# Performance work log

Hardware: AMD Instinct MI355X
Metric: run time of the kernel (lower is better)

Reference implementation:

```python
import jax, jax.numpy as jnp
import numpy as np


def setup_inputs() -> dict:
    key = jax.random.key(0)
    ks = jax.random.split(key, 9)
    B, Cr, H, W = 16, 1024, 28, 28
    Cs, Hs, Ws = 256, 25, 25  # Hs == Ws so adaptive pool == mean over width
    Ci = 512
    return {
        "x_rgb": jax.random.normal(ks[0], (B, Cr, H, W), jnp.float32),
        "x_skel": jax.random.normal(ks[1], (B, Cs, Hs, Ws), jnp.float32),
        "Wq": jax.random.normal(ks[2], (Ci, Cr), jnp.float32) * (Cr ** -0.5),
        "bq": jax.random.normal(ks[3], (Ci,), jnp.float32) * 0.01,
        "Wk": jax.random.normal(ks[4], (Ci, Cs), jnp.float32) * (Cs ** -0.5),
        "bk": jax.random.normal(ks[5], (Ci,), jnp.float32) * 0.01,
        "Wv": jax.random.normal(ks[6], (Cr, Cs), jnp.float32) * (Cs ** -0.5),
        "bv": jax.random.normal(ks[7], (Cr,), jnp.float32) * 0.01,
        "gamma": jax.random.normal(ks[8], (1,), jnp.float32) * 0.1,
    }


def reference(x_rgb, x_skel, Wq, bq, Wk, bk, Wv, bv, gamma):
    B, Cr, H, W = x_rgb.shape
    Ws = x_skel.shape[3]
    # adaptive_avg_pool2d(x_skel, (Ws, 1)) with Hs == Ws -> mean over width
    pooled = jnp.mean(x_skel, axis=3)  # [B, Cs, Ws]
    # 1x1 conv projections as matmuls
    q = jnp.einsum('ic,bchw->bihw', Wq, x_rgb) + bq[None, :, None, None]
    q = q.reshape(B, -1, H * W).transpose(0, 2, 1)          # [B, HW, Ci]
    k = jnp.einsum('ic,bcs->bis', Wk, pooled) + bk[None, :, None]  # [B, Ci, Ws]
    energy = jnp.einsum('bni,bis->bns', q, k)               # [B, HW, Ws]
    attention = jax.nn.softmax(energy, axis=-1)             # [B, HW, Ws]
    v = jnp.einsum('rc,bcs->brs', Wv, pooled) + bv[None, :, None]  # [B, Cr, Ws]
    out = jnp.einsum('brs,bns->brn', v, attention)          # [B, Cr, HW]
    out = out.reshape(B, Cr, H, W)
    return gamma[0] * out + x_rgb
```

## Files before the change

kernel.cpp:

```cpp
#include <hip/hip_runtime.h>

#define BB 16
#define CR 1024
#define HWD 784
#define HW2 392
#define CS 256
#define SSZ 25
#define SP 28
#define CI 512
#define CSPLIT 8
#define CCHUNK 128
#define RSPLIT 32
#define RCHUNK 32
#define KC 4

#define OFF_POOLED 0
#define OFF_VP     102400
#define OFF_MP     561152
#define OFF_E0     1019904
#define OFF_ATT    1020304
#define OFF_EP     1333904
#define OFF_KK     1333904
#define OFF_P      1563280

__global__ __launch_bounds__(256) void k_pool(const float* __restrict__ xs,
                                              float* __restrict__ pooled) {
    __shared__ float buf[4][400];
    int wave = threadIdx.x >> 6, lane = threadIdx.x & 63;
    int r0 = blockIdx.x * 64 + wave * 16;
    const float4* src = (const float4*)(xs + (size_t)r0 * SSZ);
    float4* b4 = (float4*)buf[wave];
    b4[lane] = src[lane];
    if (lane < 36) b4[64 + lane] = src[64 + lane];
    __syncthreads();
    if (lane < 16) {
        const float* row = buf[wave] + lane * SSZ;
        float s = 0.f;
#pragma unroll
        for (int w = 0; w < SSZ; ++w) s += row[w];
        pooled[r0 + lane] = s * (1.0f / SSZ);
    }
}

template <int NS>
__device__ __forceinline__ void proj_body(const float* __restrict__ wrow,
                                          const float* __restrict__ pb, int s0,
                                          float bias, float* __restrict__ dst,
                                          bool zpad) {
    float acc[NS];
#pragma unroll
    for (int i = 0; i < NS; ++i) acc[i] = 0.f;
    const float4* w4 = (const float4*)wrow;
#pragma unroll 4
    for (int c4 = 0; c4 < CS / 4; ++c4) {
        float4 w = w4[c4];
        const float* p = pb + c4 * 4 * SSZ + s0;
#pragma unroll
        for (int i = 0; i < NS; ++i)
            acc[i] = fmaf(w.x, p[i],
                     fmaf(w.y, p[SSZ + i],
                     fmaf(w.z, p[2 * SSZ + i],
                     fmaf(w.w, p[3 * SSZ + i], acc[i]))));
    }
#pragma unroll
    for (int i = 0; i < NS; ++i) dst[s0 + i] = acc[i] + bias;
    if (zpad) { dst[25] = 0.f; dst[26] = 0.f; dst[27] = 0.f; }
}

__global__ __launch_bounds__(256) void k_kkv(const float* __restrict__ Wk,
                                             const float* __restrict__ Wv,
                                             const float* __restrict__ bk,
                                             const float* __restrict__ bv,
                                             const float* __restrict__ pooled,
                                             float* __restrict__ kk,
                                             float* __restrict__ vp) {
    int rb = blockIdx.x >> 2, sh = blockIdx.x & 3;
    int b = blockIdx.y;
    const float* pb = pooled + (size_t)b * CS * SSZ;
    const float* wrow;
    float bias;
    float* dst;
    if (rb < 2) {
        int i = rb * 256 + threadIdx.x;
        wrow = Wk + (size_t)i * CS;
        bias = bk[i];
        dst = kk + ((size_t)b * CI + i) * SP;
    } else {
        int r = (rb - 2) * 256 + threadIdx.x;
        wrow = Wv + (size_t)r * CS;
        bias = bv[r];
        dst = vp + ((size_t)b * CR + r) * SP;
    }
    int s0 = sh * 7;
    if (sh < 3) proj_body<7>(wrow, pb, s0, bias, dst, false);
    else        proj_body<4>(wrow, pb, s0, bias, dst, true);
}

__global__ __launch_bounds__(256) void k_Mpart(const float* __restrict__ Wq,
                                               const float* __restrict__ kk,
                                               float* __restrict__ P) {
    __shared__ __align__(16) float lds[128 * 8];
    int sh = blockIdx.x, kc = blockIdx.y, b = blockIdx.z;
    int t = threadIdx.x;
    int s0 = sh * 7;
    int i0 = kc * 128;
    const float* kkb = kk + (size_t)b * CI * SP;
#pragma unroll
    for (int q = 0; q < 4; ++q) {
        int d = t + 256 * q;
        lds[d] = kkb[(size_t)(i0 + (d >> 3)) * SP + s0 + (d & 7)];
    }
    __syncthreads();

    float acc[28];
#pragma unroll
    for (int e = 0; e < 28; ++e) acc[e] = 0.f;
    const float4* lds4 = (const float4*)lds;
#pragma unroll 4
    for (int i = 0; i < 128; ++i) {
        float4 w = *(const float4*)(Wq + (size_t)(i0 + i) * CR + 4 * t);
        float4 k0 = lds4[i * 2];
        float4 k1 = lds4[i * 2 + 1];
#pragma unroll
        for (int j = 0; j < 4; ++j) {
            float wj = j == 0 ? w.x : j == 1 ? w.y : j == 2 ? w.z : w.w;
            acc[j * 7 + 0] = fmaf(wj, k0.x, acc[j * 7 + 0]);
            acc[j * 7 + 1] = fmaf(wj, k0.y, acc[j * 7 + 1]);
            acc[j * 7 + 2] = fmaf(wj, k0.z, acc[j * 7 + 2]);
            acc[j * 7 + 3] = fmaf(wj, k0.w, acc[j * 7 + 3]);
            acc[j * 7 + 4] = fmaf(wj, k1.x, acc[j * 7 + 4]);
            acc[j * 7 + 5] = fmaf(wj, k1.y, acc[j * 7 + 5]);
            acc[j * 7 + 6] = fmaf(wj, k1.z, acc[j * 7 + 6]);
        }
    }
    float* dst = P + ((((size_t)kc * BB + b) * 4 + sh) * 256 + t) * 28;
#pragma unroll
    for (int m = 0; m < 7; ++m) {
        float4 o;
        o.x = acc[4 * m + 0]; o.y = acc[4 * m + 1];
        o.z = acc[4 * m + 2]; o.w = acc[4 * m + 3];
        *(float4*)(dst + 4 * m) = o;
    }
}

__global__ __launch_bounds__(256) void k_Mred(const float* __restrict__ P,
                                              float* __restrict__ Mp) {
    int id = blockIdx.x * 256 + threadIdx.x;
    int t = id & 255, sh = (id >> 8) & 3, b = id >> 10;
    const float* p0 = P + ((((size_t)b) * 4 + sh) * 256 + t) * 28;
    const size_t PL = (size_t)BB * 4 * 256 * 28;
    float v[28];
#pragma unroll
    for (int m = 0; m < 7; ++m) {
        float4 a = *(const float4*)(p0 + 4 * m);
        float4 b1 = *(const float4*)(p0 + PL + 4 * m);
        float4 c = *(const float4*)(p0 + 2 * PL + 4 * m);
        float4 d = *(const float4*)(p0 + 3 * PL + 4 * m);
        v[4 * m + 0] = a.x + b1.x + c.x + d.x;
        v[4 * m + 1] = a.y + b1.y + c.y + d.y;
        v[4 * m + 2] = a.z + b1.z + c.z + d.z;
        v[4 * m + 3] = a.w + b1.w + c.w + d.w;
    }
    int s0 = sh * 7;
    float* mb = Mp + ((size_t)b * CR + 4 * t) * SP + s0;
#pragma unroll
    for (int j = 0; j < 4; ++j)
#pragma unroll
        for (int u = 0; u < 7; ++u)
            mb[j * SP + u] = v[j * 7 + u];
}

__global__ __launch_bounds__(64) void k_e0(const float* __restrict__ bq,
                                           const float* __restrict__ kk,
                                           float* __restrict__ e0) {
    int s = blockIdx.x, b = blockIdx.y;
    int l = threadIdx.x;
    const float* kb = kk + (size_t)b * CI * SP;
    float a = 0.f;
#pragma unroll
    for (int k = 0; k < CI / 64; ++k) {
        int i = l + 64 * k;
        a = fmaf(bq[i], kb[(size_t)i * SP + s], a);
    }
#pragma unroll
    for (int off = 32; off > 0; off >>= 1) a += __shfl_down(a, off);
    if (l == 0) e0[b * SSZ + s] = a;
}

__global__ __launch_bounds__(64) void k_energy(const float* __restrict__ xr,
                                               const float* __restrict__ Mp,
                                               float* __restrict__ Ep) {
    __shared__ float ldsM[CCHUNK * SP];
    int lane = threadIdx.x;
    int b = blockIdx.y, ch = blockIdx.z;
    int cbeg = ch * CCHUNK;
    {
        const float4* src = (const float4*)(Mp + ((size_t)b * CR + cbeg) * SP);
        float4* dst = (float4*)ldsM;
#pragma unroll
        for (int j = 0; j < 14; ++j) dst[lane + 64 * j] = src[lane + 64 * j];
    }
    __syncthreads();

    int n2 = blockIdx.x * 64 + lane;
    bool valid = n2 < HW2;
    int n2c = valid ? n2 : 0;
    const float2* x2 = (const float2*)(xr + (size_t)b * CR * HWD);

    float acc0[SP], acc1[SP];
#pragma unroll
    for (int s = 0; s < SP; ++s) { acc0[s] = 0.f; acc1[s] = 0.f; }

    for (int c = 0; c < CCHUNK; c += 4) {
        float2 xv[4];
#pragma unroll
        for (int u = 0; u < 4; ++u)
            xv[u] = x2[(size_t)(cbeg + c + u) * HW2 + n2c];
#pragma unroll
        for (int u = 0; u < 4; ++u) {
            const float4* mr = (const float4*)&ldsM[(c + u) * SP];
#pragma unroll
            for (int j = 0; j < 7; ++j) {
                float4 m = mr[j];
                acc0[4 * j + 0] = fmaf(xv[u].x, m.x, acc0[4 * j + 0]);
                acc0[4 * j + 1] = fmaf(xv[u].x, m.y, acc0[4 * j + 1]);
                acc0[4 * j + 2] = fmaf(xv[u].x, m.z, acc0[4 * j + 2]);
                acc0[4 * j + 3] = fmaf(xv[u].x, m.w, acc0[4 * j + 3]);
                acc1[4 * j + 0] = fmaf(xv[u].y, m.x, acc1[4 * j + 0]);
                acc1[4 * j + 1] = fmaf(xv[u].y, m.y, acc1[4 * j + 1]);
                acc1[4 * j + 2] = fmaf(xv[u].y, m.z, acc1[4 * j + 2]);
                acc1[4 * j + 3] = fmaf(xv[u].y, m.w, acc1[4 * j + 3]);
            }
        }
    }
    if (valid) {
        float2* ep = (float2*)Ep + ((size_t)(ch * BB + b) * SSZ) * HW2 + n2;
#pragma unroll
        for (int s = 0; s < SSZ; ++s) ep[(size_t)s * HW2] = make_float2(acc0[s], acc1[s]);
    }
}

__global__ __launch_bounds__(64) void k_softmax(const float* __restrict__ Ep,
                                                const float* __restrict__ e0,
                                                float* __restrict__ att) {
    int lane = threadIdx.x;
    int n2 = blockIdx.x * 64 + lane;
    int b = blockIdx.y;
    if (n2 >= HW2) return;
    float ex[SSZ], ey[SSZ];
#pragma unroll
    for (int s = 0; s < SSZ; ++s) { float v = e0[b * SSZ + s]; ex[s] = v; ey[s] = v; }
    const float2* ep2 = (const float2*)Ep;
    for (int ch = 0; ch < CSPLIT; ++ch) {
        const float2* ep = ep2 + ((size_t)(ch * BB + b) * SSZ) * HW2 + n2;
#pragma unroll
        for (int s = 0; s < SSZ; ++s) {
            float2 v = ep[(size_t)s * HW2];
            ex[s] += v.x; ey[s] += v.y;
        }
    }
    float mx = ex[0], my = ey[0];
#pragma unroll
    for (int s = 1; s < SSZ; ++s) { mx = fmaxf(mx, ex[s]); my = fmaxf(my, ey[s]); }
    float sx = 0.f, sy = 0.f;
#pragma unroll
    for (int s = 0; s < SSZ; ++s) {
        ex[s] = __expf(ex[s] - mx); sx += ex[s];
        ey[s] = __expf(ey[s] - my); sy += ey[s];
    }
    float ix = 1.0f / sx, iy = 1.0f / sy;
    float2* ao = (float2*)att + ((size_t)b * SSZ) * HW2 + n2;
#pragma unroll
    for (int s = 0; s < SSZ; ++s) ao[(size_t)s * HW2] = make_float2(ex[s] * ix, ey[s] * iy);
}

__global__ __launch_bounds__(64) void k_out(const float* __restrict__ xr,
                                            const float* __restrict__ vp,
                                            const float* __restrict__ att,
                                            const float* __restrict__ gamma,
                                            float* __restrict__ out) {
    __shared__ float ldsv[RCHUNK * SP];
    int lane = threadIdx.x;
    int b = blockIdx.y, rz = blockIdx.z;
    int r0 = rz * RCHUNK;
    {
        const float4* src = (const float4*)(vp + ((size_t)b * CR + r0) * SP);
        float4* dst = (float4*)ldsv;
#pragma unroll
        for (int j = 0; j < 4; ++j) {
            int idx = lane + 64 * j;
            if (idx < RCHUNK * SP / 4) dst[idx] = src[idx];
        }
    }
    __syncthreads();

    int n2 = blockIdx.x * 64 + lane;
    bool valid = n2 < HW2;
    int n2c = valid ? n2 : 0;

    float a0[SP], a1[SP];
    const float2* at2 = (const float2*)att + ((size_t)b * SSZ) * HW2 + n2c;
#pragma unroll
    for (int s = 0; s < SSZ; ++s) {
        float2 av = at2[(size_t)s * HW2];
        a0[s] = av.x; a1[s] = av.y;
    }
#pragma unroll
    for (int s = SSZ; s < SP; ++s) { a0[s] = 0.f; a1[s] = 0.f; }

    float g = gamma[0];
    const float2* x2 = (const float2*)(xr + (size_t)b * CR * HWD);
    float2* o2 = (float2*)(out + (size_t)b * CR * HWD);

#pragma unroll 4
    for (int r = 0; r < RCHUNK; ++r) {
        float2 xv = x2[(size_t)(r0 + r) * HW2 + n2c];
        float d0 = 0.f, d1 = 0.f;
        const float4* vr = (const float4*)&ldsv[r * SP];
#pragma unroll
        for (int j = 0; j < 7; ++j) {
            float4 v = vr[j];
            d0 = fmaf(v.x, a0[4 * j + 0], d0);
            d0 = fmaf(v.y, a0[4 * j + 1], d0);
            d0 = fmaf(v.z, a0[4 * j + 2], d0);
            d0 = fmaf(v.w, a0[4 * j + 3], d0);
            d1 = fmaf(v.x, a1[4 * j + 0], d1);
            d1 = fmaf(v.y, a1[4 * j + 1], d1);
            d1 = fmaf(v.z, a1[4 * j + 2], d1);
            d1 = fmaf(v.w, a1[4 * j + 3], d1);
        }
        if (valid)
            o2[(size_t)(r0 + r) * HW2 + n2] = make_float2(fmaf(g, d0, xv.x), fmaf(g, d1, xv.y));
    }
}

extern "C" void kernel_launch(void* const* d_in, const int* in_sizes, int n_in,
                              void* d_out, int out_size, void* d_ws, size_t ws_size,
                              hipStream_t stream) {
    const float* x_rgb  = (const float*)d_in[0];
    const float* x_skel = (const float*)d_in[1];
    const float* Wq     = (const float*)d_in[2];
    const float* bq     = (const float*)d_in[3];
    const float* Wk     = (const float*)d_in[4];
    const float* bk     = (const float*)d_in[5];
    const float* Wv     = (const float*)d_in[6];
    const float* bv     = (const float*)d_in[7];
    const float* gamma  = (const float*)d_in[8];
    float* out = (float*)d_out;

    float* ws     = (float*)d_ws;
    float* pooled = ws + OFF_POOLED;
    float* vp     = ws + OFF_VP;
    float* Mp     = ws + OFF_MP;
    float* e0     = ws + OFF_E0;
    float* att    = ws + OFF_ATT;
    float* Ep     = ws + OFF_EP;
    float* kk     = ws + OFF_KK;
    float* P      = ws + OFF_P;

    k_pool   <<<dim3(1600),           256, 0, stream>>>(x_skel, pooled);
    k_kkv    <<<dim3(24, 16),         256, 0, stream>>>(Wk, Wv, bk, bv, pooled, kk, vp);
    k_Mpart  <<<dim3(4, KC, 16),      256, 0, stream>>>(Wq, kk, P);
    k_Mred   <<<dim3(64),             256, 0, stream>>>(P, Mp);
    k_e0     <<<dim3(25, 16),          64, 0, stream>>>(bq, kk, e0);
    k_energy <<<dim3(7, 16, CSPLIT),   64, 0, stream>>>(x_rgb, Mp, Ep);
    k_softmax<<<dim3(7, 16),           64, 0, stream>>>(Ep, e0, att);
    k_out    <<<dim3(7, 16, RSPLIT),   64, 0, stream>>>(x_rgb, vp, att, gamma, out);
}
```

Before: 233.2 us.

## Widen energy and output kernels to float4 pixels and restructure k/v projection

The energy and output kernels now handle four pixels per lane with float4 loads and stores instead of two, and skip the padded attention columns. This raises arithmetic per LDS read and vectorizes global memory traffic, but it halves the thread count (4 pixel blocks instead of 7), which lowers parallelism. The k/v projection kernel now stages the pooled slice in shared memory and computes three weight rows times four positions per thread, reusing the pooled data across rows. The grid for that kernel becomes 14x16.

Result: slower. 254.6 us (+9.2%).

```diff
diff --git a/kernel.cpp b/kernel.cpp
--- a/kernel.cpp
+++ b/kernel.cpp
@@ -4,6 +4,7 @@
 #define CR 1024
 #define HWD 784
 #define HW2 392
+#define HW4 196
 #define CS 256
 #define SSZ 25
 #define SP 28
@@ -42,31 +43,6 @@
     }
 }
 
-template <int NS>
-__device__ __forceinline__ void proj_body(const float* __restrict__ wrow,
-                                          const float* __restrict__ pb, int s0,
-                                          float bias, float* __restrict__ dst,
-                                          bool zpad) {
-    float acc[NS];
-#pragma unroll
-    for (int i = 0; i < NS; ++i) acc[i] = 0.f;
-    const float4* w4 = (const float4*)wrow;
-#pragma unroll 4
-    for (int c4 = 0; c4 < CS / 4; ++c4) {
-        float4 w = w4[c4];
-        const float* p = pb + c4 * 4 * SSZ + s0;
-#pragma unroll
-        for (int i = 0; i < NS; ++i)
-            acc[i] = fmaf(w.x, p[i],
-                     fmaf(w.y, p[SSZ + i],
-                     fmaf(w.z, p[2 * SSZ + i],
-                     fmaf(w.w, p[3 * SSZ + i], acc[i]))));
-    }
-#pragma unroll
-    for (int i = 0; i < NS; ++i) dst[s0 + i] = acc[i] + bias;
-    if (zpad) { dst[25] = 0.f; dst[26] = 0.f; dst[27] = 0.f; }
-}
-
 __global__ __launch_bounds__(256) void k_kkv(const float* __restrict__ Wk,
                                              const float* __restrict__ Wv,
                                              const float* __restrict__ bk,
@@ -74,26 +50,61 @@
                                              const float* __restrict__ pooled,
                                              float* __restrict__ kk,
                                              float* __restrict__ vp) {
-    int rb = blockIdx.x >> 2, sh = blockIdx.x & 3;
+    __shared__ __align__(16) float ldsP[4 * 256];
+    int t = threadIdx.x;
+    int rb = blockIdx.x / 7, sh = blockIdx.x % 7;
     int b = blockIdx.y;
-    const float* pb = pooled + (size_t)b * CS * SSZ;
-    const float* wrow;
-    float bias;
-    float* dst;
-    if (rb < 2) {
-        int i = rb * 256 + threadIdx.x;
-        wrow = Wk + (size_t)i * CS;
-        bias = bk[i];
-        dst = kk + ((size_t)b * CI + i) * SP;
+    int s0 = sh * 4;
+    const float* pb = pooled + (size_t)b * CS * SSZ + t * SSZ;
+#pragma unroll
+    for (int q = 0; q < 4; ++q) {
+        int s = s0 + q;
+        ldsP[q * 256 + t] = pb[s > 24 ? 24 : s];
+    }
+    __syncthreads();
+
+    int base = rb * 768;
+    int g0 = base + t, g1 = base + 256 + t, g2 = base + 512 + t;
+    const float4* w0 = (const float4*)(g0 < 512 ? Wk + (size_t)g0 * CS
+                                                : Wv + (size_t)(g0 - 512) * CS);
+    const float4* w1 = (const float4*)(g1 < 512 ? Wk + (size_t)g1 * CS
+                                                : Wv + (size_t)(g1 - 512) * CS);
+    const float4* w2 = (const float4*)(g2 < 512 ? Wk + (size_t)g2 * CS
+                                                : Wv + (size_t)(g2 - 512) * CS);
+    float acc0[4], acc1[4], acc2[4];
+#pragma unroll
+    for (int i = 0; i < 4; ++i) { acc0[i] = 0.f; acc1[i] = 0.f; acc2[i] = 0.f; }
+
+#pragma unroll 2
+    for (int c4 = 0; c4 < CS / 4; ++c4) {
+        float4 a = w0[c4], bw = w1[c4], cw = w2[c4];
+#pragma unroll
+        for (int s = 0; s < 4; ++s) {
+            float4 p = *(const float4*)&ldsP[s * 256 + 4 * c4];
+            acc0[s] = fmaf(a.x,  p.x, fmaf(a.y,  p.y, fmaf(a.z,  p.z, fmaf(a.w,  p.w, acc0[s]))));
+            acc1[s] = fmaf(bw.x, p.x, fmaf(bw.y, p.y, fmaf(bw.z, p.z, fmaf(bw.w, p.w, acc1[s]))));
+            acc2[s] = fmaf(cw.x, p.x, fmaf(cw.y, p.y, fmaf(cw.z, p.z, fmaf(cw.w, p.w, acc2[s]))));
+        }
+    }
+
+    float bias0 = g0 < 512 ? bk[g0] : bv[g0 - 512];
+    float bias1 = g1 < 512 ? bk[g1] : bv[g1 - 512];
+    float bias2 = g2 < 512 ? bk[g2] : bv[g2 - 512];
+    float* d0 = g0 < 512 ? kk + ((size_t)b * CI + g0) * SP : vp + ((size_t)b * CR + g0 - 512) * SP;
+    float* d1 = g1 < 512 ? kk + ((size_t)b * CI + g1) * SP : vp + ((size_t)b * CR + g1 - 512) * SP;
+    float* d2 = g2 < 512 ? kk + ((size_t)b * CI + g2) * SP : vp + ((size_t)b * CR + g2 - 512) * SP;
+    if (sh < 6) {
+#pragma unroll
+        for (int i = 0; i < 4; ++i) {
+            d0[s0 + i] = acc0[i] + bias0;
+            d1[s0 + i] = acc1[i] + bias1;
+            d2[s0 + i] = acc2[i] + bias2;
+        }
     } else {
-        int r = (rb - 2) * 256 + threadIdx.x;
-        wrow = Wv + (size_t)r * CS;
-        bias = bv[r];
-        dst = vp + ((size_t)b * CR + r) * SP;
-    }
-    int s0 = sh * 7;
-    if (sh < 3) proj_body<7>(wrow, pb, s0, bias, dst, false);
-    else        proj_body<4>(wrow, pb, s0, bias, dst, true);
+        d0[24] = acc0[0] + bias0; d0[25] = 0.f; d0[26] = 0.f; d0[27] = 0.f;
+        d1[24] = acc1[0] + bias1; d1[25] = 0.f; d1[26] = 0.f; d1[27] = 0.f;
+        d2[24] = acc2[0] + bias2; d2[25] = 0.f; d2[26] = 0.f; d2[27] = 0.f;
+    }
 }
 
 __global__ __launch_bounds__(256) void k_Mpart(const float* __restrict__ Wq,
@@ -202,41 +213,43 @@
     }
     __syncthreads();
 
-    int n2 = blockIdx.x * 64 + lane;
-    bool valid = n2 < HW2;
-    int n2c = valid ? n2 : 0;
-    const float2* x2 = (const float2*)(xr + (size_t)b * CR * HWD);
-
-    float acc0[SP], acc1[SP];
-#pragma unroll
-    for (int s = 0; s < SP; ++s) { acc0[s] = 0.f; acc1[s] = 0.f; }
-
-    for (int c = 0; c < CCHUNK; c += 4) {
-        float2 xv[4];
-#pragma unroll
-        for (int u = 0; u < 4; ++u)
-            xv[u] = x2[(size_t)(cbeg + c + u) * HW2 + n2c];
-#pragma unroll
-        for (int u = 0; u < 4; ++u) {
+    int n4 = blockIdx.x * 64 + lane;
+    bool valid = n4 < HW4;
+    int n4c = valid ? n4 : 0;
+    const float4* x4 = (const float4*)xr + (size_t)b * CR * HW4;
+
+    float4 acc[SSZ];
+#pragma unroll
+    for (int s = 0; s < SSZ; ++s) acc[s] = make_float4(0.f, 0.f, 0.f, 0.f);
+
+    for (int c = 0; c < CCHUNK; c += 2) {
+        float4 xv0 = x4[(size_t)(cbeg + c) * HW4 + n4c];
+        float4 xv1 = x4[(size_t)(cbeg + c + 1) * HW4 + n4c];
+#pragma unroll
+        for (int u = 0; u < 2; ++u) {
+            float4 xv = u == 0 ? xv0 : xv1;
             const float4* mr = (const float4*)&ldsM[(c + u) * SP];
 #pragma unroll
             for (int j = 0; j < 7; ++j) {
                 float4 m = mr[j];
-                acc0[4 * j + 0] = fmaf(xv[u].x, m.x, acc0[4 * j + 0]);
-                acc0[4 * j + 1] = fmaf(xv[u].x, m.y, acc0[4 * j + 1]);
-                acc0[4 * j + 2] = fmaf(xv[u].x, m.z, acc0[4 * j + 2]);
-                acc0[4 * j + 3] = fmaf(xv[u].x, m.w, acc0[4 * j + 3]);
-                acc1[4 * j + 0] = fmaf(xv[u].y, m.x, acc1[4 * j + 0]);
-                acc1[4 * j + 1] = fmaf(xv[u].y, m.y, acc1[4 * j + 1]);
-                acc1[4 * j + 2] = fmaf(xv[u].y, m.z, acc1[4 * j + 2]);
-                acc1[4 * j + 3] = fmaf(xv[u].y, m.w, acc1[4 * j + 3]);
+#pragma unroll
+                for (int k = 0; k < 4; ++k) {
+                    int s = 4 * j + k;
+                    if (s < SSZ) {
+                        float mv = k == 0 ? m.x : k == 1 ? m.y : k == 2 ? m.z : m.w;
+                        acc[s].x = fmaf(xv.x, mv, acc[s].x);
+                        acc[s].y = fmaf(xv.y, mv, acc[s].y);
+                        acc[s].z = fmaf(xv.z, mv, acc[s].z);
+                        acc[s].w = fmaf(xv.w, mv, acc[s].w);
+                    }
+                }
             }
         }
     }
     if (valid) {
-        float2* ep = (float2*)Ep + ((size_t)(ch * BB + b) * SSZ) * HW2 + n2;
-#pragma unroll
-        for (int s = 0; s < SSZ; ++s) ep[(size_t)s * HW2] = make_float2(acc0[s], acc1[s]);
+        float4* ep = (float4*)Ep + ((size_t)(ch * BB + b) * SSZ) * HW4 + n4;
+#pragma unroll
+        for (int s = 0; s < SSZ; ++s) ep[(size_t)s * HW4] = acc[s];
     }
 }
 
@@ -294,43 +307,43 @@
     }
     __syncthreads();
 
-    int n2 = blockIdx.x * 64 + lane;
-    bool valid = n2 < HW2;
-    int n2c = valid ? n2 : 0;
-
-    float a0[SP], a1[SP];
-    const float2* at2 = (const float2*)att + ((size_t)b * SSZ) * HW2 + n2c;
-#pragma unroll
-    for (int s = 0; s < SSZ; ++s) {
-        float2 av = at2[(size_t)s * HW2];
-        a0[s] = av.x; a1[s] = av.y;
-    }
-#pragma unroll
-    for (int s = SSZ; s < SP; ++s) { a0[s] = 0.f; a1[s] = 0.f; }
+    int n4 = blockIdx.x * 64 + lane;
+    bool valid = n4 < HW4;
+    int n4c = valid ? n4 : 0;
+
+    float4 a[SSZ];
+    const float4* at4 = (const float4*)att + ((size_t)b * SSZ) * HW4 + n4c;
+#pragma unroll
+    for (int s = 0; s < SSZ; ++s) a[s] = at4[(size_t)s * HW4];
 
     float g = gamma[0];
-    const float2* x2 = (const float2*)(xr + (size_t)b * CR * HWD);
-    float2* o2 = (float2*)(out + (size_t)b * CR * HWD);
-
-#pragma unroll 4
+    const float4* x4 = (const float4*)xr + (size_t)b * CR * HW4;
+    float4* o4 = (float4*)out + (size_t)b * CR * HW4;
+
+#pragma unroll 2
     for (int r = 0; r < RCHUNK; ++r) {
-        float2 xv = x2[(size_t)(r0 + r) * HW2 + n2c];
-        float d0 = 0.f, d1 = 0.f;
+        float4 xv = x4[(size_t)(r0 + r) * HW4 + n4c];
+        float4 d = make_float4(0.f, 0.f, 0.f, 0.f);
         const float4* vr = (const float4*)&ldsv[r * SP];
 #pragma unroll
         for (int j = 0; j < 7; ++j) {
             float4 v = vr[j];
-            d0 = fmaf(v.x, a0[4 * j + 0], d0);
-            d0 = fmaf(v.y, a0[4 * j + 1], d0);
-            d0 = fmaf(v.z, a0[4 * j + 2], d0);
-            d0 = fmaf(v.w, a0[4 * j + 3], d0);
-            d1 = fmaf(v.x, a1[4 * j + 0], d1);
-            d1 = fmaf(v.y, a1[4 * j + 1], d1);
-            d1 = fmaf(v.z, a1[4 * j + 2], d1);
-            d1 = fmaf(v.w, a1[4 * j + 3], d1);
+#pragma unroll
+            for (int k = 0; k < 4; ++k) {
+                int s = 4 * j + k;
+                if (s < SSZ) {
+                    float vv = k == 0 ? v.x : k == 1 ? v.y : k == 2 ? v.z : v.w;
+                    d.x = fmaf(vv, a[s].x, d.x);
+                    d.y = fmaf(vv, a[s].y, d.y);
+                    d.z = fmaf(vv, a[s].z, d.z);
+                    d.w = fmaf(vv, a[s].w, d.w);
+                }
+            }
         }
         if (valid)
-            o2[(size_t)(r0 + r) * HW2 + n2] = make_float2(fmaf(g, d0, xv.x), fmaf(g, d1, xv.y));
+            o4[(size_t)(r0 + r) * HW4 + n4] =
+                make_float4(fmaf(g, d.x, xv.x), fmaf(g, d.y, xv.y),
+                            fmaf(g, d.z, xv.z), fmaf(g, d.w, xv.w));
     }
 }
 
@@ -359,11 +372,11 @@
     float* P      = ws + OFF_P;
 
     k_pool   <<<dim3(1600),           256, 0, stream>>>(x_skel, pooled);
-    k_kkv    <<<dim3(24, 16),         256, 0, stream>>>(Wk, Wv, bk, bv, pooled, kk, vp);
+    k_kkv    <<<dim3(14, 16),         256, 0, stream>>>(Wk, Wv, bk, bv, pooled, kk, vp);
     k_Mpart  <<<dim3(4, KC, 16),      256, 0, stream>>>(Wq, kk, P);
     k_Mred   <<<dim3(64),             256, 0, stream>>>(P, Mp);
     k_e0     <<<dim3(25, 16),          64, 0, stream>>>(bq, kk, e0);
-    k_energy <<<dim3(7, 16, CSPLIT),   64, 0, stream>>>(x_rgb, Mp, Ep);
+    k_energy <<<dim3(4, 16, CSPLIT),   64, 0, stream>>>(x_rgb, Mp, Ep);
     k_softmax<<<dim3(7, 16),           64, 0, stream>>>(Ep, e0, att);
-    k_out    <<<dim3(7, 16, RSPLIT),   64, 0, stream>>>(x_rgb, vp, att, gamma, out);
-}
+    k_out    <<<dim3(4, 16, RSPLIT),   64, 0, stream>>>(x_rgb, vp, att, gamma, out);
+}
```
